# Optimization experiments

Measured on AMD Instinct MI355X. Metric: run time of the kernel, lower is better.

Reference implementation:

```python
import jax, jax.numpy as jnp
import numpy as np
import math

HEADS = 8
HIDDEN = 512
HEAD_DIM = HIDDEN // HEADS
BATCH = 16
N = 512
ALPHA = 1.0 / math.sqrt(HEAD_DIM)


def setup_inputs() -> dict:
    key = jax.random.key(0)
    ks = jax.random.split(key, 6)
    stdv_qkv = 1.0 / math.sqrt(HEAD_DIM)
    stdv_o = 1.0 / math.sqrt(HIDDEN)
    return {
        "x": jax.random.normal(ks[0], (BATCH, N, HIDDEN), dtype=jnp.float32),
        "edge": jax.random.normal(ks[1], (HEADS, BATCH, N, N), dtype=jnp.float32),
        "Wq": jax.random.uniform(ks[2], (HEADS, HIDDEN, HEAD_DIM), jnp.float32, -stdv_qkv, stdv_qkv),
        "Wk": jax.random.uniform(ks[3], (HEADS, HIDDEN, HEAD_DIM), jnp.float32, -stdv_qkv, stdv_qkv),
        "Wv": jax.random.uniform(ks[4], (HEADS, HIDDEN, HEAD_DIM), jnp.float32, -stdv_qkv, stdv_qkv),
        "Wo": jax.random.uniform(ks[5], (HIDDEN, HIDDEN), jnp.float32, -stdv_o, stdv_o),
    }


def reference(x, edge, Wq, Wk, Wv, Wo):
    # per-head projections: x [b,n,h] x W [g,h,d] -> [g,b,n,d]
    Q = jnp.einsum("bnh,ghd->gbnd", x, Wq)
    K = jnp.einsum("bnh,ghd->gbnd", x, Wk)
    V = jnp.einsum("bnh,ghd->gbnd", x, Wv)
    # edge-biased attention scores [g,b,n,n]
    S = edge + ALPHA * jnp.einsum("gbnd,gbmd->gbnm", Q, K)
    S = jax.nn.softmax(S, axis=-1)
    # attend and merge heads: [g,b,n,d] -> [b,n,g*d]
    o = jnp.einsum("gbnm,gbmd->bngd", S, V)
    o = o.reshape(o.shape[0], o.shape[1], -1)
    return o @ Wo
```

## Files before the change

kernel.cpp:

```cpp
#include <hip/hip_runtime.h>

typedef __bf16 bf16;
typedef __bf16 bf16x4 __attribute__((ext_vector_type(4)));
typedef __bf16 bf16x8 __attribute__((ext_vector_type(8)));
typedef float f32x4 __attribute__((ext_vector_type(4)));

#define ALPHA_ 0.125f


__device__ __forceinline__ void gload16(const void* g, void* l) {
  __builtin_amdgcn_global_load_lds((__attribute__((address_space(1))) void*)(g),
                                   (__attribute__((address_space(3))) void*)(l),
                                   16, 0, 0);
}

__global__ void cast_x_kernel(const float* __restrict__ x, bf16* __restrict__ xb) {
  int i = blockIdx.x * 256 + threadIdx.x;
  float4 v = ((const float4*)x)[i];
  bf16x4 o = {(bf16)v.x, (bf16)v.y, (bf16)v.z, (bf16)v.w};
  ((bf16x4*)xb)[i] = o;
}

__global__ void prep_w_kernel(const float* __restrict__ Wq, const float* __restrict__ Wk,
                              const float* __restrict__ Wv, bf16* __restrict__ wcat) {
  int i = blockIdx.x * 256 + threadIdx.x;
  int h = i & 511, j = i >> 9;
  int qkv = j >> 9, g = (j >> 6) & 7, d = j & 63;
  const float* W = (qkv == 0) ? Wq : ((qkv == 1) ? Wk : Wv);
  wcat[i] = (bf16)W[((g << 9) + h) * 64 + d];
}

__global__ void prep_wo_kernel(const float* __restrict__ Wo, bf16* __restrict__ wot) {
  int i = blockIdx.x * 256 + threadIdx.x;
  int k = i & 511, n = i >> 9;
  wot[i] = (bf16)Wo[(k << 9) + n];
}

template <int MODE>
__global__ __launch_bounds__(256, 2) void gemm_bt_kernel(
    const bf16* __restrict__ A, const bf16* __restrict__ Bt, int Kdim, int Ndim,
    float* __restrict__ Cf, bf16* __restrict__ Qo, bf16* __restrict__ Ko,
    bf16* __restrict__ Vto) {
  __shared__ bf16 lA[128 * 32];
  __shared__ bf16 lB[128 * 32];
  const int t = threadIdx.x;
  const int w = t >> 6;
  const int lane = t & 63;
  const int lhi = lane >> 4, llo = lane & 15;
  const int m0 = blockIdx.y * 128, n0 = blockIdx.x * 128;
  const int wr = (w >> 1) * 64, wc = (w & 1) * 64;

  f32x4 acc[4][4] = {};
  const int nkt = Kdim >> 5;
  for (int kt = 0; kt < nkt; ++kt) {
#pragma unroll
    for (int c = 0; c < 2; ++c) {
      int u = c * 256 + t;
      const bf16* ga = A + (size_t)(m0 + (u >> 2)) * Kdim + kt * 32 + (u & 3) * 8;
      gload16(ga, &lA[c * 2048 + w * 512]);
      const bf16* gb = Bt + (size_t)(n0 + (u >> 2)) * Kdim + kt * 32 + (u & 3) * 8;
      gload16(gb, &lB[c * 2048 + w * 512]);
    }
    __syncthreads();
    bf16x8 af[4], bfr[4];
#pragma unroll
    for (int i = 0; i < 4; ++i) {
      af[i] = *(const bf16x8*)&lA[(wr + i * 16 + llo) * 32 + lhi * 8];
      bfr[i] = *(const bf16x8*)&lB[(wc + i * 16 + llo) * 32 + lhi * 8];
    }
#pragma unroll
    for (int i = 0; i < 4; ++i)
#pragma unroll
      for (int j = 0; j < 4; ++j)
        acc[i][j] = __builtin_amdgcn_mfma_f32_16x16x32_bf16(af[i], bfr[j], acc[i][j], 0, 0, 0);
    __syncthreads();
  }

#pragma unroll
  for (int i = 0; i < 4; ++i) {
    int row = m0 + wr + i * 16 + lhi * 4;
#pragma unroll
    for (int j = 0; j < 4; ++j) {
      int col = n0 + wc + j * 16 + llo;
#pragma unroll
      for (int r = 0; r < 4; ++r) {
        float v = acc[i][j][r];
        int rr = row + r;
        if (MODE == 0) {
          int qkv = col >> 9, g = (col >> 6) & 7, d = col & 63;
          bf16 bv = (bf16)v;
          if (qkv == 0)
            Qo[((size_t)g * 8192 + rr) * 64 + d] = bv;
          else if (qkv == 1)
            Ko[((size_t)g * 8192 + rr) * 64 + d] = bv;
          else {
            int b = rr >> 9, n = rr & 511;
            Vto[(((size_t)g * 16 + b) * 64 + d) * 512 + n] = bv;
          }
        } else {
          Cf[(size_t)rr * Ndim + col] = v;
        }
      }
    }
  }
}

__global__ __launch_bounds__(256, 4) void attn_kernel(
    const bf16* __restrict__ Qa, const bf16* __restrict__ Ka,
    const bf16* __restrict__ Vta, const float* __restrict__ edge,
    bf16* __restrict__ Oatt) {
  __shared__ bf16 lK[64 * 64];
  __shared__ bf16 lV[64 * 64];
  const int t = threadIdx.x, w = t >> 6, lane = t & 63;
  const int lhi = lane >> 4, llo = lane & 15;
  const int qt = blockIdx.x, b = blockIdx.y, g = blockIdx.z;
  const int q0 = qt * 64 + w * 16;
  const bf16* Qg = Qa + ((size_t)g * 8192 + b * 512) * 64;
  const bf16* Kg = Ka + ((size_t)g * 8192 + b * 512) * 64;
  const bf16* Vg = Vta + ((size_t)g * 16 + b) * (64 * 512);
  const float* eg = edge + ((size_t)g * 16 + b) * (512 * 512);

  bf16x8 qf[2];
#pragma unroll
  for (int ks = 0; ks < 2; ++ks)
    qf[ks] = *(const bf16x8*)(Qg + (size_t)(q0 + llo) * 64 + ks * 32 + lhi * 8);

  f32x4 oacc[4] = {};
  float mrow = -3e38f, lrow = 0.f;

  const int r0c = t >> 3, c0c = (t & 7) * 8;
  const int r1c = (256 + t) >> 3, c1c = c0c;

  bf16x8 kcur[2], vcur[2], knxt[2], vnxt[2];
  kcur[0] = *(const bf16x8*)(Kg + (size_t)r0c * 64 + c0c);
  kcur[1] = *(const bf16x8*)(Kg + (size_t)r1c * 64 + c1c);
  vcur[0] = *(const bf16x8*)(Vg + (size_t)r0c * 512 + c0c);
  vcur[1] = *(const bf16x8*)(Vg + (size_t)r1c * 512 + c1c);

  for (int it = 0; it < 8; ++it) {
    const int kv0 = it * 64;
    *(bf16x8*)&lK[(r0c * 64 + c0c) ^ ((r0c & 7) << 3)] = kcur[0];
    *(bf16x8*)&lK[(r1c * 64 + c1c) ^ ((r1c & 7) << 3)] = kcur[1];
    *(bf16x8*)&lV[(r0c * 64 + c0c) ^ ((r0c & 7) << 3)] = vcur[0];
    *(bf16x8*)&lV[(r1c * 64 + c1c) ^ ((r1c & 7) << 3)] = vcur[1];
    if (it < 7) {
      const int kvn = kv0 + 64;
      knxt[0] = *(const bf16x8*)(Kg + (size_t)(kvn + r0c) * 64 + c0c);
      knxt[1] = *(const bf16x8*)(Kg + (size_t)(kvn + r1c) * 64 + c1c);
      vnxt[0] = *(const bf16x8*)(Vg + (size_t)r0c * 512 + kvn + c0c);
      vnxt[1] = *(const bf16x8*)(Vg + (size_t)r1c * 512 + kvn + c1c);
    }
    f32x4 ef[4];
#pragma unroll
    for (int ni = 0; ni < 4; ++ni)
      ef[ni] = *(const f32x4*)(eg + (size_t)(q0 + llo) * 512 + kv0 + ni * 16 + lhi * 4);

    asm volatile("s_waitcnt lgkmcnt(0)" ::: "memory");
    __builtin_amdgcn_sched_barrier(0);
    __builtin_amdgcn_s_barrier();
    __builtin_amdgcn_sched_barrier(0);

    f32x4 sc[4] = {};
#pragma unroll
    for (int ks = 0; ks < 2; ++ks) {
      bf16x8 kf[4];
#pragma unroll
      for (int ni = 0; ni < 4; ++ni) {
        int row = ni * 16 + llo;
        kf[ni] = *(const bf16x8*)&lK[(row * 64 + ks * 32 + lhi * 8) ^ ((row & 7) << 3)];
      }
#pragma unroll
      for (int ni = 0; ni < 4; ++ni)
        sc[ni] = __builtin_amdgcn_mfma_f32_16x16x32_bf16(kf[ni], qf[ks], sc[ni], 0, 0, 0);
    }

    float mx = -3e38f;
#pragma unroll
    for (int ni = 0; ni < 4; ++ni)
#pragma unroll
      for (int r = 0; r < 4; ++r) {
        float sv = fmaf(ALPHA_, sc[ni][r], ef[ni][r]);
        sc[ni][r] = sv;
        mx = fmaxf(mx, sv);
      }
    mx = fmaxf(mx, __shfl_xor(mx, 16));
    mx = fmaxf(mx, __shfl_xor(mx, 32));
    float mnew = fmaxf(mrow, mx);
    float s = __expf(mrow - mnew);
    mrow = mnew;
    float rsum = 0.f;
#pragma unroll
    for (int ni = 0; ni < 4; ++ni)
#pragma unroll
      for (int r = 0; r < 4; ++r) {
        float p = __expf(sc[ni][r] - mnew);
        sc[ni][r] = p;
        rsum += p;
      }
    rsum += __shfl_xor(rsum, 16);
    rsum += __shfl_xor(rsum, 32);
    lrow = lrow * s + rsum;

#pragma unroll
    for (int r = 0; r < 4; ++r) {
      float sq = __shfl(s, (lane & 48) | (lhi * 4 + r));
#pragma unroll
      for (int nc = 0; nc < 4; ++nc) oacc[nc][r] *= sq;
    }

#pragma unroll
    for (int ks2 = 0; ks2 < 2; ++ks2) {
      const int n0 = ks2 * 2, n1 = n0 + 1;
      unsigned xa, xb, ya, yb;
      asm("v_cvt_pk_bf16_f32 %0, %1, %2" : "=v"(xa) : "v"(sc[n0][0]), "v"(sc[n0][1]));
      asm("v_cvt_pk_bf16_f32 %0, %1, %2" : "=v"(xb) : "v"(sc[n0][2]), "v"(sc[n0][3]));
      asm("v_cvt_pk_bf16_f32 %0, %1, %2" : "=v"(ya) : "v"(sc[n1][0]), "v"(sc[n1][1]));
      asm("v_cvt_pk_bf16_f32 %0, %1, %2" : "=v"(yb) : "v"(sc[n1][2]), "v"(sc[n1][3]));
      asm("v_permlane32_swap_b32 %0, %1" : "+v"(xa), "+v"(ya));
      asm("v_permlane16_swap_b32 %0, %1" : "+v"(xa), "+v"(ya));
      asm("v_permlane32_swap_b32 %0, %1" : "+v"(xb), "+v"(yb));
      asm("v_permlane16_swap_b32 %0, %1" : "+v"(xb), "+v"(yb));
      union { unsigned wd[4]; bf16x8 v; } fu;
      fu.wd[0] = xa; fu.wd[1] = xb; fu.wd[2] = ya; fu.wd[3] = yb;
      bf16x8 pf = fu.v;

      bf16x8 vf[4];
#pragma unroll
      for (int nc = 0; nc < 4; ++nc) {
        int row = nc * 16 + llo;
        vf[nc] = *(const bf16x8*)&lV[(row * 64 + ks2 * 32 + lhi * 8) ^ ((row & 7) << 3)];
      }
#pragma unroll
      for (int nc = 0; nc < 4; ++nc)
        oacc[nc] = __builtin_amdgcn_mfma_f32_16x16x32_bf16(pf, vf[nc], oacc[nc], 0, 0, 0);
    }

    __builtin_amdgcn_sched_barrier(0);
    __builtin_amdgcn_s_barrier();
    __builtin_amdgcn_sched_barrier(0);

    if (it < 7) {
      kcur[0] = knxt[0]; kcur[1] = knxt[1];
      vcur[0] = vnxt[0]; vcur[1] = vnxt[1];
    }
  }

  float rcpl = 1.0f / lrow;
#pragma unroll
  for (int r = 0; r < 4; ++r) {
    float lr = __shfl(rcpl, (lane & 48) | (lhi * 4 + r));
    int qrow = q0 + lhi * 4 + r;
#pragma unroll
    for (int nc = 0; nc < 4; ++nc) {
      float ov = oacc[nc][r] * lr;
      Oatt[((size_t)b * 512 + qrow) * 512 + g * 64 + nc * 16 + llo] = (bf16)ov;
    }
  }
}

extern "C" void kernel_launch(void* const* d_in, const int* in_sizes, int n_in,
                              void* d_out, int out_size, void* d_ws, size_t ws_size,
                              hipStream_t stream) {
  (void)in_sizes; (void)n_in; (void)out_size; (void)ws_size;
  const float* x = (const float*)d_in[0];
  const float* edge = (const float*)d_in[1];
  const float* Wq = (const float*)d_in[2];
  const float* Wk = (const float*)d_in[3];
  const float* Wv = (const float*)d_in[4];
  const float* Wo = (const float*)d_in[5];
  float* out = (float*)d_out;

  char* ws = (char*)d_ws;
  bf16* xb   = (bf16*)(ws + 0);
  bf16* wcat = (bf16*)(ws + 8388608);
  bf16* wot  = (bf16*)(ws + 9961472);
  bf16* Qa   = (bf16*)(ws + 10485760);
  bf16* Ka   = (bf16*)(ws + 18874368);
  bf16* Vta  = (bf16*)(ws + 27262976);
  bf16* Oatt = (bf16*)(ws + 35651584);

  cast_x_kernel<<<4096, 256, 0, stream>>>(x, xb);
  prep_w_kernel<<<3072, 256, 0, stream>>>(Wq, Wk, Wv, wcat);
  prep_wo_kernel<<<1024, 256, 0, stream>>>(Wo, wot);

  gemm_bt_kernel<0><<<dim3(12, 64), 256, 0, stream>>>(xb, wcat, 512, 1536,
                                                      nullptr, Qa, Ka, Vta);
  attn_kernel<<<dim3(8, 16, 8), 256, 0, stream>>>(Qa, Ka, Vta, edge, Oatt);
  gemm_bt_kernel<1><<<dim3(4, 64), 256, 0, stream>>>(Oatt, wot, 512, 512,
                                                     out, nullptr, nullptr, nullptr);
}
```

Before: 108.1 us.

## Double-buffer K/V in LDS via direct global-to-LDS loads and prefetch edge

The attention kernel now keeps two LDS buffers for K and V and fills the next tile with asynchronous global_load_lds while the current tile is computed, instead of staging through registers and storing to LDS each iteration. The XOR swizzle moves to the global-address side so that it matches the existing LDS read pattern. The edge-bias tile for the next iteration is also loaded one step ahead, with vmcnt-based waits. MFMA sections are wrapped in s_setprio. This aims to hide global-memory latency and cut register pressure and LDS store instructions, at the cost of doubled LDS use, which may limit occupancy.

```diff
diff --git a/kernel.cpp b/kernel.cpp
--- a/kernel.cpp
+++ b/kernel.cpp
@@ -7,6 +7,9 @@
 
 #define ALPHA_ 0.125f
 
+
+struct FalseT { static constexpr bool value = false; };
+struct TrueT  { static constexpr bool value = true;  };
 
 __device__ __forceinline__ void gload16(const void* g, void* l) {
   __builtin_amdgcn_global_load_lds((__attribute__((address_space(1))) void*)(g),
@@ -109,8 +112,8 @@
     const bf16* __restrict__ Qa, const bf16* __restrict__ Ka,
     const bf16* __restrict__ Vta, const float* __restrict__ edge,
     bf16* __restrict__ Oatt) {
-  __shared__ bf16 lK[64 * 64];
-  __shared__ bf16 lV[64 * 64];
+  __shared__ bf16 lK[2][64 * 64];
+  __shared__ bf16 lV[2][64 * 64];
   const int t = threadIdx.x, w = t >> 6, lane = t & 63;
   const int lhi = lane >> 4, llo = lane & 15;
   const int qt = blockIdx.x, b = blockIdx.y, g = blockIdx.z;
@@ -128,51 +131,58 @@
   f32x4 oacc[4] = {};
   float mrow = -3e38f, lrow = 0.f;
 
-  const int r0c = t >> 3, c0c = (t & 7) * 8;
-  const int r1c = (256 + t) >> 3, c1c = c0c;
-
-  bf16x8 kcur[2], vcur[2], knxt[2], vnxt[2];
-  kcur[0] = *(const bf16x8*)(Kg + (size_t)r0c * 64 + c0c);
-  kcur[1] = *(const bf16x8*)(Kg + (size_t)r1c * 64 + c1c);
-  vcur[0] = *(const bf16x8*)(Vg + (size_t)r0c * 512 + c0c);
-  vcur[1] = *(const bf16x8*)(Vg + (size_t)r1c * 512 + c1c);
-
-  for (int it = 0; it < 8; ++it) {
+  const int r0 = t >> 3;
+  const int r1 = r0 + 32;
+  const int cs = (((t & 7) ^ (r0 & 7)) << 3);
+
+  f32x4 ef[4], efn[4];
+
+  gload16(Kg + (size_t)r0 * 64 + cs, &lK[0][w * 512]);
+  gload16(Kg + (size_t)r1 * 64 + cs, &lK[0][2048 + w * 512]);
+  gload16(Vg + (size_t)r0 * 512 + cs, &lV[0][w * 512]);
+  gload16(Vg + (size_t)r1 * 512 + cs, &lV[0][2048 + w * 512]);
+#pragma unroll
+  for (int ni = 0; ni < 4; ++ni)
+    ef[ni] = *(const f32x4*)(eg + (size_t)(q0 + llo) * 512 + ni * 16 + lhi * 4);
+
+  auto iter_body = [&](int it, auto LASTC) {
+    constexpr bool LAST = decltype(LASTC)::value;
     const int kv0 = it * 64;
-    *(bf16x8*)&lK[(r0c * 64 + c0c) ^ ((r0c & 7) << 3)] = kcur[0];
-    *(bf16x8*)&lK[(r1c * 64 + c1c) ^ ((r1c & 7) << 3)] = kcur[1];
-    *(bf16x8*)&lV[(r0c * 64 + c0c) ^ ((r0c & 7) << 3)] = vcur[0];
-    *(bf16x8*)&lV[(r1c * 64 + c1c) ^ ((r1c & 7) << 3)] = vcur[1];
-    if (it < 7) {
+    const int cur = it & 1;
+    if constexpr (!LAST) {
+      const int nxt = cur ^ 1;
       const int kvn = kv0 + 64;
-      knxt[0] = *(const bf16x8*)(Kg + (size_t)(kvn + r0c) * 64 + c0c);
-      knxt[1] = *(const bf16x8*)(Kg + (size_t)(kvn + r1c) * 64 + c1c);
-      vnxt[0] = *(const bf16x8*)(Vg + (size_t)r0c * 512 + kvn + c0c);
-      vnxt[1] = *(const bf16x8*)(Vg + (size_t)r1c * 512 + kvn + c1c);
-    }
-    f32x4 ef[4];
-#pragma unroll
-    for (int ni = 0; ni < 4; ++ni)
-      ef[ni] = *(const f32x4*)(eg + (size_t)(q0 + llo) * 512 + kv0 + ni * 16 + lhi * 4);
-
-    asm volatile("s_waitcnt lgkmcnt(0)" ::: "memory");
+      gload16(Kg + (size_t)(kvn + r0) * 64 + cs, &lK[nxt][w * 512]);
+      gload16(Kg + (size_t)(kvn + r1) * 64 + cs, &lK[nxt][2048 + w * 512]);
+      gload16(Vg + (size_t)r0 * 512 + kvn + cs, &lV[nxt][w * 512]);
+      gload16(Vg + (size_t)r1 * 512 + kvn + cs, &lV[nxt][2048 + w * 512]);
+#pragma unroll
+      for (int ni = 0; ni < 4; ++ni)
+        efn[ni] = *(const f32x4*)(eg + (size_t)(q0 + llo) * 512 + kvn + ni * 16 + lhi * 4);
+    }
+    if constexpr (!LAST)
+      asm volatile("s_waitcnt vmcnt(8)" ::: "memory");
+    else
+      asm volatile("s_waitcnt vmcnt(0)" ::: "memory");
     __builtin_amdgcn_sched_barrier(0);
     __builtin_amdgcn_s_barrier();
     __builtin_amdgcn_sched_barrier(0);
 
     f32x4 sc[4] = {};
+    __builtin_amdgcn_s_setprio(1);
 #pragma unroll
     for (int ks = 0; ks < 2; ++ks) {
       bf16x8 kf[4];
 #pragma unroll
       for (int ni = 0; ni < 4; ++ni) {
         int row = ni * 16 + llo;
-        kf[ni] = *(const bf16x8*)&lK[(row * 64 + ks * 32 + lhi * 8) ^ ((row & 7) << 3)];
+        kf[ni] = *(const bf16x8*)&lK[cur][(row * 64 + ks * 32 + lhi * 8) ^ ((row & 7) << 3)];
       }
 #pragma unroll
       for (int ni = 0; ni < 4; ++ni)
         sc[ni] = __builtin_amdgcn_mfma_f32_16x16x32_bf16(kf[ni], qf[ks], sc[ni], 0, 0, 0);
     }
+    __builtin_amdgcn_s_setprio(0);
 
     float mx = -3e38f;
 #pragma unroll
@@ -208,6 +218,7 @@
       for (int nc = 0; nc < 4; ++nc) oacc[nc][r] *= sq;
     }
 
+    __builtin_amdgcn_s_setprio(1);
 #pragma unroll
     for (int ks2 = 0; ks2 < 2; ++ks2) {
       const int n0 = ks2 * 2, n1 = n0 + 1;
@@ -228,22 +239,25 @@
 #pragma unroll
       for (int nc = 0; nc < 4; ++nc) {
         int row = nc * 16 + llo;
-        vf[nc] = *(const bf16x8*)&lV[(row * 64 + ks2 * 32 + lhi * 8) ^ ((row & 7) << 3)];
+        vf[nc] = *(const bf16x8*)&lV[cur][(row * 64 + ks2 * 32 + lhi * 8) ^ ((row & 7) << 3)];
       }
 #pragma unroll
       for (int nc = 0; nc < 4; ++nc)
         oacc[nc] = __builtin_amdgcn_mfma_f32_16x16x32_bf16(pf, vf[nc], oacc[nc], 0, 0, 0);
     }
-
-    __builtin_amdgcn_sched_barrier(0);
-    __builtin_amdgcn_s_barrier();
-    __builtin_amdgcn_sched_barrier(0);
-
-    if (it < 7) {
-      kcur[0] = knxt[0]; kcur[1] = knxt[1];
-      vcur[0] = vnxt[0]; vcur[1] = vnxt[1];
-    }
-  }
+    __builtin_amdgcn_s_setprio(0);
+
+    if constexpr (!LAST) {
+      __builtin_amdgcn_sched_barrier(0);
+      __builtin_amdgcn_s_barrier();
+      __builtin_amdgcn_sched_barrier(0);
+#pragma unroll
+      for (int ni = 0; ni < 4; ++ni) ef[ni] = efn[ni];
+    }
+  };
+
+  for (int it = 0; it < 7; ++it) iter_body(it, FalseT{});
+  iter_body(7, TrueT{});
 
   float rcpl = 1.0f / lrow;
 #pragma unroll
```

Result: no change. 106.8 us (-1.2%).
